# Performance work log

Measured on AMD Instinct MI355X. Metric: run time of the kernel, lower is better.

The kernel has to match this reference:

```python
import jax, jax.numpy as jnp
import numpy as np

LAMBDA_FREQ = 0.1
LOWPASS_RATIO = 0.25
EPS_RATIO = 0.05
H_SPATIAL = 128
W_SPATIAL = 128


def _crps_pointwise(pred, target):
    # pred: (B, M, C, G); target: (B, C, G)
    M = pred.shape[1]
    eps = EPS_RATIO / M
    mae = jnp.abs(pred - target[:, None]).mean(axis=1)  # (B, C, G)
    term1 = mae.mean()
    # pairwise |p_i - p_j|: (B, M, M, C, G); diagonal is exactly 0 already
    pairwise = jnp.abs(pred[:, :, None] - pred[:, None, :])
    spread = pairwise.sum(axis=2) / (M - 1)  # (B, M, C, G)
    term2 = spread.mean() * (1.0 - eps)
    return term1 - 0.5 * term2


def _lowpass_fft(x):
    # x: (B, M, C, H, W) -> complex (B, M, C, H, W//2+1), low-pass masked
    X = jnp.fft.rfft2(x, axes=(-2, -1))
    Hf, Wf = X.shape[-2], X.shape[-1]
    cut_h = max(int(Hf * LOWPASS_RATIO), 1)
    cut_w = max(int(Wf * LOWPASS_RATIO), 1)
    mask = jnp.zeros((Hf, Wf), dtype=bool).at[:cut_h, :cut_w].set(True)
    return X * mask


def setup_inputs() -> dict:
    key = jax.random.key(0)
    k1, k2 = jax.random.split(key)
    target = jax.random.normal(k1, (8, 3, H_SPATIAL, W_SPATIAL), dtype=jnp.float32)
    output = jax.random.normal(k2, (8, 16, 3, H_SPATIAL, W_SPATIAL), dtype=jnp.float32)
    return {"target": target, "output": output}


def reference(target, output):
    B, M, C = output.shape[0], output.shape[1], output.shape[2]
    target_flat = target.reshape(B, C, -1)           # (B, C, G)
    output_flat = output.reshape(B, M, C, -1)        # (B, M, C, G)
    crps_p = _crps_pointwise(output_flat, target_flat)

    out_fft = _lowpass_fft(output).reshape(B, M, C, -1)             # (B, M, C, Gf)
    tgt_fft = _lowpass_fft(target[:, None]).reshape(B, C, -1)       # (B, C, Gf)
    crps_f = _crps_pointwise(jnp.abs(out_fft), jnp.abs(tgt_fft))

    return crps_p + LAMBDA_FREQ * crps_f
```

## Files before the change

### kernel.cpp

```cpp
#include <hip/hip_runtime.h>
#include <math.h>

#define NB 8
#define NM 16
#define NC 3
#define NH 128
#define NW 128
#define NG (NH * NW)
#define NGF (NH * (NW / 2 + 1))
#define NKH 32
#define NKW 16
#define NK (NKH * NKW)
#define N_PRED_IMG (NB * NM * NC)
#define N_IMG (N_PRED_IMG + NB * NC)

#define PT_BLOCKS 384
#define FQ_BLOCKS 48

#define WS_PP_OFF  0
#define WS_FP_OFF  6144
#define WS_CTR_OFF 6912
#define WS_MAG_OFF 7168

#define PI_F 3.14159265358979323846f

__device__ __forceinline__ float2 cmul(float2 a, float2 b) {
  return make_float2(a.x * b.x - a.y * b.y, a.x * b.y + a.y * b.x);
}

__global__ __launch_bounds__(256) void fused_main_kernel(
    const float* __restrict__ pred,
    const float* __restrict__ tgt,
    double2* __restrict__ pp,
    float* __restrict__ mag,
    unsigned* __restrict__ ctr) {
  __shared__ float4 xs4[32 * 33];
  __shared__ float2 Yl[NH * NKW];
  __shared__ float ls1[4], ls2[4];

  const int t = threadIdx.x;
  const int blk = blockIdx.x;

  if (blk < PT_BLOCKS) {
    if (blk == 0 && t == 0) *ctr = 0;
    int i4 = (blk * 256 + t) * 4;
    int b = i4 / (NC * NG);
    int cg = i4 - b * (NC * NG);
    const float* base = pred + (size_t)b * (NM * NC * NG) + cg;
    float4 tv = *(const float4*)&tgt[i4];
    float4 p[NM];
#pragma unroll
    for (int m = 0; m < NM; ++m)
      p[m] = *(const float4*)&base[(size_t)m * (NC * NG)];

    float s1 = 0.f, s2 = 0.f;
#pragma unroll
    for (int m = 0; m < NM; ++m)
      s1 += fabsf(p[m].x - tv.x) + fabsf(p[m].y - tv.y) +
            fabsf(p[m].z - tv.z) + fabsf(p[m].w - tv.w);
#pragma unroll
    for (int m = 0; m < NM; ++m)
#pragma unroll
      for (int j = m + 1; j < NM; ++j)
        s2 += fabsf(p[m].x - p[j].x) + fabsf(p[m].y - p[j].y) +
              fabsf(p[m].z - p[j].z) + fabsf(p[m].w - p[j].w);

    for (int off = 32; off > 0; off >>= 1) {
      s1 += __shfl_down(s1, off);
      s2 += __shfl_down(s2, off);
    }
    if ((t & 63) == 0) { ls1[t >> 6] = s1; ls2[t >> 6] = s2; }
    __syncthreads();
    if (t == 0) {
      double a = 0.0, c = 0.0;
#pragma unroll
      for (int w = 0; w < 4; ++w) { a += (double)ls1[w]; c += (double)ls2[w]; }
      pp[blk] = make_double2(a, c);
    }
    return;
  }

  const int img = blk - PT_BLOCKS;
  const float* src = (img < N_PRED_IMG)
                         ? pred + (size_t)img * NG
                         : tgt + (size_t)(img - N_PRED_IMG) * NG;
  const float4* src4 = (const float4*)src;

  const int kw = t & 15, r2 = t >> 4;
  float sw, cw;
  sincosf(-2.0f * PI_F * (float)kw / 128.0f, &sw, &cw);
  const float2 stepw = make_float2(cw, sw);

  for (int c = 0; c < 4; ++c) {
#pragma unroll
    for (int j = 0; j < 4; ++j) {
      int p = j * 256 + t;
      float4 v = src4[c * 1024 + p];
      xs4[(p >> 5) * 33 + (p & 31)] = v;
    }
    __syncthreads();

    float ax1 = 0.f, ay1 = 0.f, ax2 = 0.f, ay2 = 0.f;
    float2 rt = make_float2(1.f, 0.f);
    const float4* rowA = &xs4[r2 * 33];
    const float4* rowB = &xs4[(r2 + 16) * 33];
#pragma unroll 8
    for (int w4 = 0; w4 < 32; ++w4) {
      float4 a = rowA[w4];
      float4 bb = rowB[w4];
      ax1 = fmaf(a.x, rt.x, ax1); ay1 = fmaf(a.x, rt.y, ay1);
      ax2 = fmaf(bb.x, rt.x, ax2); ay2 = fmaf(bb.x, rt.y, ay2);
      rt = cmul(rt, stepw);
      ax1 = fmaf(a.y, rt.x, ax1); ay1 = fmaf(a.y, rt.y, ay1);
      ax2 = fmaf(bb.y, rt.x, ax2); ay2 = fmaf(bb.y, rt.y, ay2);
      rt = cmul(rt, stepw);
      ax1 = fmaf(a.z, rt.x, ax1); ay1 = fmaf(a.z, rt.y, ay1);
      ax2 = fmaf(bb.z, rt.x, ax2); ay2 = fmaf(bb.z, rt.y, ay2);
      rt = cmul(rt, stepw);
      ax1 = fmaf(a.w, rt.x, ax1); ay1 = fmaf(a.w, rt.y, ay1);
      ax2 = fmaf(bb.w, rt.x, ax2); ay2 = fmaf(bb.w, rt.y, ay2);
      rt = cmul(rt, stepw);
    }
    Yl[(c * 32 + r2) * NKW + kw] = make_float2(ax1, ay1);
    Yl[(c * 32 + r2 + 16) * NKW + kw] = make_float2(ax2, ay2);
    __syncthreads();
  }

  const int kh = t >> 3, kw2 = (t & 7) * 2;
  float sh, ch;
  sincosf(-2.0f * PI_F * (float)kh / 128.0f, &sh, &ch);
  const float2 steph = make_float2(ch, sh);
  float axA = 0.f, ayA = 0.f, axB = 0.f, ayB = 0.f;
  float2 rt = make_float2(1.f, 0.f);
#pragma unroll 8
  for (int h = 0; h < NH; ++h) {
    float4 y2 = *(const float4*)&Yl[h * NKW + kw2];
    axA = fmaf(y2.x, rt.x, fmaf(-y2.y, rt.y, axA));
    ayA = fmaf(y2.x, rt.y, fmaf(y2.y, rt.x, ayA));
    axB = fmaf(y2.z, rt.x, fmaf(-y2.w, rt.y, axB));
    ayB = fmaf(y2.z, rt.y, fmaf(y2.w, rt.x, ayB));
    rt = cmul(rt, steph);
  }
  float* mo = mag + (size_t)img * NK;
  mo[kh * NKW + kw2] = sqrtf(axA * axA + ayA * ayA);
  mo[kh * NKW + kw2 + 1] = sqrtf(axB * axB + ayB * ayB);
}

__global__ __launch_bounds__(256) void crps_freq_final_kernel(
    const float* __restrict__ mag,
    const double2* __restrict__ pp,
    double2* __restrict__ fp,
    unsigned* __restrict__ ctr,
    float* __restrict__ out) {
  const int tid = threadIdx.x;
  int i = blockIdx.x * 256 + tid;
  int b = i / (NC * NK);
  int rem = i - b * (NC * NK);
  const float* pb = mag + (size_t)b * (NM * NC * NK) + rem;
  float t = mag[(size_t)N_PRED_IMG * NK + (size_t)b * (NC * NK) + rem];
  float p[NM];
#pragma unroll
  for (int m = 0; m < NM; ++m) p[m] = pb[(size_t)m * (NC * NK)];
  float s1 = 0.f, s2 = 0.f;
#pragma unroll
  for (int m = 0; m < NM; ++m) s1 += fabsf(p[m] - t);
#pragma unroll
  for (int m = 0; m < NM; ++m)
#pragma unroll
    for (int j = m + 1; j < NM; ++j) s2 += fabsf(p[m] - p[j]);
  for (int off = 32; off > 0; off >>= 1) {
    s1 += __shfl_down(s1, off);
    s2 += __shfl_down(s2, off);
  }
  __shared__ float ls1[4], ls2[4];
  __shared__ int sLast;
  if ((tid & 63) == 0) { ls1[tid >> 6] = s1; ls2[tid >> 6] = s2; }
  __syncthreads();
  if (tid == 0) {
    double a = 0.0, c = 0.0;
#pragma unroll
    for (int w = 0; w < 4; ++w) { a += (double)ls1[w]; c += (double)ls2[w]; }
    fp[blockIdx.x] = make_double2(a, c);
    __threadfence();
    unsigned old = atomicAdd(ctr, 1u);
    sLast = (old == FQ_BLOCKS - 1);
  }
  __syncthreads();
  if (!sLast) return;
  __threadfence();

  double s1p = 0.0, s2p = 0.0, s1f = 0.0, s2f = 0.0;
  for (int j = tid; j < PT_BLOCKS; j += 256) {
    double2 v = pp[j]; s1p += v.x; s2p += v.y;
  }
  if (tid < FQ_BLOCKS) { double2 v = fp[tid]; s1f += v.x; s2f += v.y; }
  for (int off = 32; off > 0; off >>= 1) {
    s1p += __shfl_down(s1p, off);
    s2p += __shfl_down(s2p, off);
    s1f += __shfl_down(s1f, off);
    s2f += __shfl_down(s2f, off);
  }
  __shared__ double l[4][4];
  if ((tid & 63) == 0) {
    int w = tid >> 6;
    l[w][0] = s1p; l[w][1] = s2p; l[w][2] = s1f; l[w][3] = s2f;
  }
  __syncthreads();
  if (tid == 0) {
    double a0 = 0, a1 = 0, a2 = 0, a3 = 0;
#pragma unroll
    for (int w = 0; w < 4; ++w) {
      a0 += l[w][0]; a1 += l[w][1]; a2 += l[w][2]; a3 += l[w][3];
    }
    const double Bd = NB, Md = NM, Cd = NC, Gd = NG, Gfd = NGF;
    const double eps = 0.05 / Md;
    double term1_p = a0 / (Bd * Cd * Gd * Md);
    double term2_p = (1.0 - eps) * 2.0 * a1 / ((Md - 1.0) * Bd * Md * Cd * Gd);
    double crps_p = term1_p - 0.5 * term2_p;
    double term1_f = a2 / (Bd * Cd * Gfd * Md);
    double term2_f = (1.0 - eps) * 2.0 * a3 / ((Md - 1.0) * Bd * Md * Cd * Gfd);
    double crps_f = term1_f - 0.5 * term2_f;
    out[0] = (float)(crps_p + 0.1 * crps_f);
  }
}

extern "C" void kernel_launch(void* const* d_in, const int* in_sizes, int n_in,
                              void* d_out, int out_size, void* d_ws, size_t ws_size,
                              hipStream_t stream) {
  (void)in_sizes; (void)n_in; (void)out_size; (void)ws_size;
  const float* tgt = (const float*)d_in[0];
  const float* pred = (const float*)d_in[1];
  float* out = (float*)d_out;

  char* ws = (char*)d_ws;
  double2* pp = (double2*)(ws + WS_PP_OFF);
  double2* fp = (double2*)(ws + WS_FP_OFF);
  unsigned* ctr = (unsigned*)(ws + WS_CTR_OFF);
  float* mag = (float*)(ws + WS_MAG_OFF);

  fused_main_kernel<<<PT_BLOCKS + N_IMG, 256, 0, stream>>>(pred, tgt, pp, mag, ctr);
  crps_freq_final_kernel<<<FQ_BLOCKS, 256, 0, stream>>>(mag, pp, fp, ctr, out);
}
```

Baseline: 104.3 us.

## Compute row DFT directly from global memory with 8 rows per thread

```diff
diff --git a/kernel.cpp b/kernel.cpp
--- a/kernel.cpp
+++ b/kernel.cpp
@@ -34,7 +34,6 @@
     double2* __restrict__ pp,
     float* __restrict__ mag,
     unsigned* __restrict__ ctr) {
-  __shared__ float4 xs4[32 * 33];
   __shared__ float2 Yl[NH * NKW];
   __shared__ float ls1[4], ls2[4];
 
@@ -86,60 +85,64 @@
                          : tgt + (size_t)(img - N_PRED_IMG) * NG;
   const float4* src4 = (const float4*)src;
 
-  const int kw = t & 15, r2 = t >> 4;
+  const int kw = t & 15, rg = t >> 4;
   float sw, cw;
   sincosf(-2.0f * PI_F * (float)kw / 128.0f, &sw, &cw);
   const float2 stepw = make_float2(cw, sw);
 
-  for (int c = 0; c < 4; ++c) {
-#pragma unroll
-    for (int j = 0; j < 4; ++j) {
-      int p = j * 256 + t;
-      float4 v = src4[c * 1024 + p];
-      xs4[(p >> 5) * 33 + (p & 31)] = v;
-    }
-    __syncthreads();
-
-    float ax1 = 0.f, ay1 = 0.f, ax2 = 0.f, ay2 = 0.f;
-    float2 rt = make_float2(1.f, 0.f);
-    const float4* rowA = &xs4[r2 * 33];
-    const float4* rowB = &xs4[(r2 + 16) * 33];
-#pragma unroll 8
-    for (int w4 = 0; w4 < 32; ++w4) {
-      float4 a = rowA[w4];
-      float4 bb = rowB[w4];
-      ax1 = fmaf(a.x, rt.x, ax1); ay1 = fmaf(a.x, rt.y, ay1);
-      ax2 = fmaf(bb.x, rt.x, ax2); ay2 = fmaf(bb.x, rt.y, ay2);
-      rt = cmul(rt, stepw);
-      ax1 = fmaf(a.y, rt.x, ax1); ay1 = fmaf(a.y, rt.y, ay1);
-      ax2 = fmaf(bb.y, rt.x, ax2); ay2 = fmaf(bb.y, rt.y, ay2);
-      rt = cmul(rt, stepw);
-      ax1 = fmaf(a.z, rt.x, ax1); ay1 = fmaf(a.z, rt.y, ay1);
-      ax2 = fmaf(bb.z, rt.x, ax2); ay2 = fmaf(bb.z, rt.y, ay2);
-      rt = cmul(rt, stepw);
-      ax1 = fmaf(a.w, rt.x, ax1); ay1 = fmaf(a.w, rt.y, ay1);
-      ax2 = fmaf(bb.w, rt.x, ax2); ay2 = fmaf(bb.w, rt.y, ay2);
-      rt = cmul(rt, stepw);
-    }
-    Yl[(c * 32 + r2) * NKW + kw] = make_float2(ax1, ay1);
-    Yl[(c * 32 + r2 + 16) * NKW + kw] = make_float2(ax2, ay2);
-    __syncthreads();
-  }
+  float ax[8], ay[8];
+#pragma unroll
+  for (int j = 0; j < 8; ++j) { ax[j] = 0.f; ay[j] = 0.f; }
+  const float4* rp[8];
+#pragma unroll
+  for (int j = 0; j < 8; ++j) rp[j] = src4 + (size_t)(rg + 16 * j) * 32;
+
+  float2 rt = make_float2(1.f, 0.f);
+#pragma unroll 2
+  for (int w4 = 0; w4 < 32; ++w4) {
+    float4 v[8];
+#pragma unroll
+    for (int j = 0; j < 8; ++j) v[j] = rp[j][w4];
+#pragma unroll
+    for (int j = 0; j < 8; ++j) {
+      ax[j] = fmaf(v[j].x, rt.x, ax[j]); ay[j] = fmaf(v[j].x, rt.y, ay[j]);
+    }
+    rt = cmul(rt, stepw);
+#pragma unroll
+    for (int j = 0; j < 8; ++j) {
+      ax[j] = fmaf(v[j].y, rt.x, ax[j]); ay[j] = fmaf(v[j].y, rt.y, ay[j]);
+    }
+    rt = cmul(rt, stepw);
+#pragma unroll
+    for (int j = 0; j < 8; ++j) {
+      ax[j] = fmaf(v[j].z, rt.x, ax[j]); ay[j] = fmaf(v[j].z, rt.y, ay[j]);
+    }
+    rt = cmul(rt, stepw);
+#pragma unroll
+    for (int j = 0; j < 8; ++j) {
+      ax[j] = fmaf(v[j].w, rt.x, ax[j]); ay[j] = fmaf(v[j].w, rt.y, ay[j]);
+    }
+    rt = cmul(rt, stepw);
+  }
+#pragma unroll
+  for (int j = 0; j < 8; ++j)
+    Yl[(rg + 16 * j) * NKW + kw] = make_float2(ax[j], ay[j]);
+  __syncthreads();
 
   const int kh = t >> 3, kw2 = (t & 7) * 2;
   float sh, ch;
   sincosf(-2.0f * PI_F * (float)kh / 128.0f, &sh, &ch);
   const float2 steph = make_float2(ch, sh);
   float axA = 0.f, ayA = 0.f, axB = 0.f, ayB = 0.f;
-  float2 rt = make_float2(1.f, 0.f);
+  float2 rtc = make_float2(1.f, 0.f);
 #pragma unroll 8
   for (int h = 0; h < NH; ++h) {
     float4 y2 = *(const float4*)&Yl[h * NKW + kw2];
-    axA = fmaf(y2.x, rt.x, fmaf(-y2.y, rt.y, axA));
-    ayA = fmaf(y2.x, rt.y, fmaf(y2.y, rt.x, ayA));
-    axB = fmaf(y2.z, rt.x, fmaf(-y2.w, rt.y, axB));
-    ayB = fmaf(y2.z, rt.y, fmaf(y2.w, rt.x, ayB));
-    rt = cmul(rt, steph);
+    axA = fmaf(y2.x, rtc.x, fmaf(-y2.y, rtc.y, axA));
+    ayA = fmaf(y2.x, rtc.y, fmaf(y2.y, rtc.x, ayA));
+    axB = fmaf(y2.z, rtc.x, fmaf(-y2.w, rtc.y, axB));
+    ayB = fmaf(y2.z, rtc.y, fmaf(y2.w, rtc.x, ayB));
+    rtc = cmul(rtc, steph);
   }
   float* mo = mag + (size_t)img * NK;
   mo[kh * NKW + kw2] = sqrtf(axA * axA + ayA * ayA);
```

Measured after the change: 101.5 us. 1.03x faster.
